# Kernel optimization log

Hardware: AMD Instinct MI355X
Metric: run time of the kernel (lower is better)

Reference implementation:

```python
import jax, jax.numpy as jnp
import numpy as np
from jax import lax

DIM = 64
BF = 2          # branching_factor
NUM_HEADS = 8
N_POS = 4096


def _expm(A, order=12, squarings=8):
    """Differentiable matrix exponential via scaling-and-squaring + Horner Taylor.
    Faithful substitute for torch.matrix_exp on skew-symmetric inputs."""
    d = A.shape[-1]
    I = jnp.eye(d, dtype=A.dtype)
    A = A / (2.0 ** squarings)
    E = I
    for k in range(order, 0, -1):
        E = I + jnp.matmul(A, E) / k
    for _ in range(squarings):
        E = jnp.matmul(E, E)
    return E


def _path_words_np(positions, bf):
    """Replicates create_paths + pad_sequence(padding_value=bf): tree path digits
    of node `pos` (root->leaf), right-padded with bf to the max actual length."""
    paths = []
    for p in positions:
        digs = []
        idx = int(p)
        while idx > 0:
            digs.append((idx - 1) % bf)
            idx = (idx - 1) // bf
        paths.append(digs[::-1] if p > 0 else [])
    T = max(1, max(len(p) for p in paths))
    out = np.full((len(paths), T), bf, dtype=np.int32)
    for i, p in enumerate(paths):
        out[i, :len(p)] = p
    return out


def setup_inputs() -> dict:
    key = jax.random.key(0)
    raw = jax.random.uniform(key, (BF * NUM_HEADS + 1, DIM, DIM), dtype=jnp.float32)
    # mimics torch.rand(...).softmax(-1).cumsum(-1) init of _primitives
    primitives_raw = jnp.cumsum(jax.nn.softmax(raw, axis=-1), axis=-1)
    positions = np.arange(N_POS)
    path_words = jnp.asarray(_path_words_np(positions, BF))  # [N, T] int32
    return {"primitives_raw": primitives_raw, "path_words": path_words}


def reference(primitives_raw, path_words):
    # primitives = matrix_exp(P - P^T)
    hermitian = primitives_raw - jnp.swapaxes(primitives_raw, -1, -2)
    primitives = _expm(hermitian)                      # [BF*H+1, d, d]
    d = primitives.shape[-1]
    I = jnp.eye(d, dtype=primitives.dtype)

    # linear(x, W) = x @ W.T; padding ids BF and BF+1 act as identity (no update)
    ext = jnp.concatenate(
        [jnp.swapaxes(primitives[:BF], -1, -2), jnp.broadcast_to(I, (2, d, d))],
        axis=0)                                        # [BF+2, d, d]

    n = path_words.shape[0]
    M0 = jnp.broadcast_to(I, (n, d, d))

    def body(M, w):  # w: [n] branch ids at this tree depth
        return jnp.einsum('nij,njk->nik', M, ext[w]), None

    M, _ = lax.scan(body, M0, path_words.T)            # fold over path depth
    maps = M[:, None]                                  # [n, 1, d, d]

    # create_steps: tree distance via common-prefix lengths
    pm = path_words != BF + 1                          # point mask [n, T]
    mask = pm[:, None, :] & pm[None, :, :]             # [n, n, T]
    eq = path_words[:, None, :] == path_words[None, :, :]
    common = lax.associative_scan(jnp.logical_and, eq, axis=-1) & mask
    lens = pm.sum(-1)
    steps = lens[:, None] + lens[None, :] - 2 * common.sum(-1).astype(lens.dtype)
    return maps, steps
```

## Files before the change

kernel.cpp:

```cpp
#include <hip/hip_runtime.h>


#define NPOS 4096
#define TLEN 12

typedef __attribute__((ext_vector_type(8))) short short8;
typedef __attribute__((ext_vector_type(4))) float f32x4;

__device__ __forceinline__ unsigned short f2bf(float f) {
  union { float f; unsigned u; } v; v.f = f;
  unsigned r = v.u + 0x7fffu + ((v.u >> 16) & 1u);
  return (unsigned short)(r >> 16);
}

__device__ __forceinline__ void mm64v(const float P[64][68], const float B[64][64],
                                      float acc[4][4], int r0, int c0) {
#pragma unroll 4
  for (int k0 = 0; k0 < 64; k0 += 4) {
    float a[4][4], bb[4][4];
#pragma unroll
    for (int i = 0; i < 4; ++i) {
      const float4 t = *reinterpret_cast<const float4*>(&P[r0 + i][k0]);
      a[i][0] = t.x; a[i][1] = t.y; a[i][2] = t.z; a[i][3] = t.w;
    }
#pragma unroll
    for (int kk = 0; kk < 4; ++kk) {
      const float4 t = *reinterpret_cast<const float4*>(&B[k0 + kk][c0]);
      bb[kk][0] = t.x; bb[kk][1] = t.y; bb[kk][2] = t.z; bb[kk][3] = t.w;
    }
#pragma unroll
    for (int i = 0; i < 4; ++i)
#pragma unroll
      for (int kk = 0; kk < 4; ++kk)
#pragma unroll
        for (int j = 0; j < 4; ++j) acc[i][j] += a[i][kk] * bb[kk][j];
  }
}

__device__ __forceinline__ float step_val(unsigned a, unsigned b) {
  const unsigned x = a ^ b;
  const int cp = x ? (__builtin_clz(x) >> 1) : TLEN;
  return (float)(2 * TLEN - 2 * cp);
}

__global__ __launch_bounds__(256) void expm_steps_kernel(
    const float* __restrict__ raw, const unsigned* __restrict__ keys,
    unsigned short* __restrict__ tabR, unsigned short* __restrict__ tabT,
    float* __restrict__ steps_out) {
  __shared__ float P[64][68];
  __shared__ float Bs[64][64];
  const int t = threadIdx.x;

  if (blockIdx.x >= 2) {
    const int b = (int)blockIdx.x - 2;
    const int i = b >> 2;
    const int j0 = ((b & 3) << 10) | (t << 2);
    const unsigned ki = keys[i];
    const uint4 kj = *reinterpret_cast<const uint4*>(&keys[j0]);
    float4 r;
    r.x = step_val(ki, kj.x);
    r.y = step_val(ki, kj.y);
    r.z = step_val(ki, kj.z);
    r.w = step_val(ki, kj.w);
    *reinterpret_cast<float4*>(&steps_out[(size_t)i * NPOS + j0]) = r;
    return;
  }

  const int d = blockIdx.x;
  const int r0 = (t >> 4) << 2, c0 = (t & 15) << 2;
#pragma unroll
  for (int i = 0; i < 16; ++i) {
    const int idx = (i << 8) | t;
    const int r = idx >> 6, c = idx & 63;
    const float a = (raw[d * 4096 + r * 64 + c] - raw[d * 4096 + c * 64 + r]) * (1.0f / 256.0f);
    P[r][c] = a;
    Bs[r][c] = ((r == c) ? 1.0f : 0.0f) + a * 0.2f;
  }
  __syncthreads();

  for (int k = 4; k >= 1; --k) {
    float acc[4][4] = {};
    mm64v(P, Bs, acc, r0, c0);
    __syncthreads();
    const float inv = 1.0f / (float)k;
#pragma unroll
    for (int i = 0; i < 4; ++i)
#pragma unroll
      for (int j = 0; j < 4; ++j) {
        const int r = r0 + i, c = c0 + j;
        Bs[r][c] = ((r == c) ? 1.0f : 0.0f) + acc[i][j] * inv;
      }
    __syncthreads();
  }

  for (int s = 0; s < 8; ++s) {
#pragma unroll
    for (int i = 0; i < 16; ++i) {
      const int idx = (i << 8) | t;
      P[idx >> 6][idx & 63] = Bs[idx >> 6][idx & 63];
    }
    __syncthreads();
    float acc[4][4] = {};
    mm64v(P, Bs, acc, r0, c0);
    __syncthreads();
#pragma unroll
    for (int i = 0; i < 4; ++i)
      *reinterpret_cast<float4*>(&Bs[r0 + i][c0]) =
          make_float4(acc[i][0], acc[i][1], acc[i][2], acc[i][3]);
    __syncthreads();
  }

  unsigned short* oR = tabR + (size_t)(1 + d) * 4096;
  unsigned short* oT = tabT + (size_t)(1 + d) * 4096;
#pragma unroll
  for (int i = 0; i < 16; ++i) {
    const int idx = (i << 8) | t;
    const int r = idx >> 6, c = idx & 63;
    oR[idx] = f2bf(Bs[c][r]);
    oT[idx] = f2bf(Bs[r][c]);
  }
  if (d == 0) {
#pragma unroll
    for (int i = 0; i < 16; ++i) {
      const int idx = (i << 8) | t;
      const int r = idx >> 6, c = idx & 63;
      const unsigned short v = (r == c) ? (unsigned short)0x3F80 : (unsigned short)0;
      tabR[idx] = v;
      tabT[idx] = v;
    }
  }
}

__device__ __forceinline__ void mfma64(const unsigned short* __restrict__ X,
                                       const unsigned short* __restrict__ Yt,
                                       f32x4 acc[4], int wv, int l) {
  const int row = l & 15, g = l >> 4;
  short8 a[2], b[4][2];
#pragma unroll
  for (int q = 0; q < 2; ++q)
    a[q] = *reinterpret_cast<const short8*>(X + (((16 * wv + row) << 6) | (q << 5) | (g << 3)));
#pragma unroll
  for (int c = 0; c < 4; ++c)
#pragma unroll
    for (int q = 0; q < 2; ++q)
      b[c][q] = *reinterpret_cast<const short8*>(Yt + (((16 * c + row) << 6) | (q << 5) | (g << 3)));
#pragma unroll
  for (int c = 0; c < 4; ++c) {
    acc[c] = __builtin_amdgcn_mfma_f32_16x16x32_bf16(a[0], b[c][0], acc[c], 0, 0, 0);
    acc[c] = __builtin_amdgcn_mfma_f32_16x16x32_bf16(a[1], b[c][1], acc[c], 0, 0, 0);
  }
}

__global__ __launch_bounds__(256) void pair_kernel(unsigned short* __restrict__ tabR,
                                                   unsigned short* __restrict__ tabT,
                                                   int mode) {
  const int bid = blockIdx.x;
  int xe, ye, oe;
  if (mode == 0) {
    xe = 1 + (bid >> 1); ye = 1 + (bid & 1); oe = 3 + bid;
  } else if (mode == 1) {
    if (bid < 8) { xe = 3 + (bid >> 1); ye = 1 + (bid & 1); oe = 7 + bid; }
    else { const int v = bid - 8; xe = 3 + (v >> 2); ye = 3 + (v & 3); oe = 15 + v; }
  } else {
    if (bid < 32) { xe = 15 + (bid >> 1); ye = 1 + (bid & 1); oe = 31 + bid; }
    else { const int v = bid - 32; xe = 15 + (v >> 2); ye = 3 + (v & 3); oe = 63 + v; }
  }
  const int wv = threadIdx.x >> 6, l = threadIdx.x & 63;
  f32x4 acc[4] = {f32x4{0,0,0,0}, f32x4{0,0,0,0}, f32x4{0,0,0,0}, f32x4{0,0,0,0}};
  mfma64(tabR + (size_t)xe * 4096, tabT + (size_t)ye * 4096, acc, wv, l);
  unsigned short* oR = tabR + (size_t)oe * 4096;
  unsigned short* oT = tabT + (size_t)oe * 4096;
  const int row = l & 15, g = l >> 4;
#pragma unroll
  for (int c = 0; c < 4; ++c)
#pragma unroll
    for (int r = 0; r < 4; ++r) {
      const unsigned short v = f2bf(acc[c][r]);
      const int rr = 16 * wv + 4 * g + r, cc = 16 * c + row;
      oR[rr * 64 + cc] = v;
      oT[cc * 64 + rr] = v;
    }
}

__global__ __launch_bounds__(256) void maps_kernel(const int* __restrict__ pw,
                                                   const unsigned short* __restrict__ tabR,
                                                   const unsigned short* __restrict__ tabT,
                                                   float* __restrict__ out) {
  const int n = blockIdx.x;
  int v1 = 0, l1 = 0, v2 = 0, l2 = 0;
#pragma unroll
  for (int tt = 0; tt < 6; ++tt) {
    const int w = pw[n * TLEN + tt];
    if (w < 2) { v1 = (v1 << 1) | w; ++l1; }
  }
#pragma unroll
  for (int tt = 6; tt < 12; ++tt) {
    const int w = pw[n * TLEN + tt];
    if (w < 2) { v2 = (v2 << 1) | w; ++l2; }
  }
  const int wv = threadIdx.x >> 6, l = threadIdx.x & 63;
  f32x4 acc[4] = {f32x4{0,0,0,0}, f32x4{0,0,0,0}, f32x4{0,0,0,0}, f32x4{0,0,0,0}};
  mfma64(tabR + (size_t)((1 << l1) - 1 + v1) * 4096,
         tabT + (size_t)((1 << l2) - 1 + v2) * 4096, acc, wv, l);
  float* O = out + (size_t)n * 4096;
  const int row = l & 15, g = l >> 4;
#pragma unroll
  for (int c = 0; c < 4; ++c)
#pragma unroll
    for (int r = 0; r < 4; ++r)
      O[((16 * wv + 4 * g + r) << 6) | (16 * c + row)] = acc[c][r];
}

__global__ __launch_bounds__(256) void keys_kernel(const int* __restrict__ pw,
                                                   unsigned* __restrict__ keys) {
  const int n = blockIdx.x * 256 + threadIdx.x;
  unsigned k = 0;
#pragma unroll
  for (int tt = 0; tt < TLEN; ++tt) k = (k << 2) | (unsigned)pw[n * TLEN + tt];
  keys[n] = k << 8;
}

extern "C" void kernel_launch(void* const* d_in, const int* in_sizes, int n_in,
                              void* d_out, int out_size, void* d_ws, size_t ws_size,
                              hipStream_t stream) {
  const float* raw = (const float*)d_in[0];
  const int* pw = (const int*)d_in[1];
  float* out = (float*)d_out;

  unsigned short* tabR = (unsigned short*)d_ws;
  unsigned short* tabT = tabR + (size_t)127 * 4096;
  unsigned* keys = (unsigned*)((char*)d_ws + (2u << 20));

  keys_kernel<<<NPOS / 256, 256, 0, stream>>>(pw, keys);
  expm_steps_kernel<<<2 + NPOS * 4, 256, 0, stream>>>(raw, keys, tabR, tabT,
                                                      out + (size_t)NPOS * 4096);
  pair_kernel<<<4, 256, 0, stream>>>(tabR, tabT, 0);
  pair_kernel<<<24, 256, 0, stream>>>(tabR, tabT, 1);
  pair_kernel<<<96, 256, 0, stream>>>(tabR, tabT, 2);
  maps_kernel<<<NPOS, 256, 0, stream>>>(pw, tabR, tabT, out);
}
```

Baseline: 185.5 us.

## Rework expm with Paterson-Stockmeyer, merge pair kernels, coalesce map stores

Several changes land together. The matrix exponential now uses fewer squarings (6 instead of 8) with a Paterson-Stockmeyer style evaluation of the degree-12 Taylor polynomial built from A and A^2, and uses packed float2 FMAs. The three level-by-level pair kernels become one 124-block kernel in which each block recomputes its own product chain from the two base primitives, which removes two launches and the inter-kernel dependency. The maps kernel stages its result in shared memory so it can write output with coalesced float4 stores. The serial expm chain and per-launch overhead are the targets, at the cost of redundant chained MFMA work in the pairs kernel and slightly changed numerics.

Result: slower. 199.1 us (+7.3%).

```diff
diff --git a/kernel.cpp b/kernel.cpp
--- a/kernel.cpp
+++ b/kernel.cpp
@@ -6,6 +6,7 @@
 
 typedef __attribute__((ext_vector_type(8))) short short8;
 typedef __attribute__((ext_vector_type(4))) float f32x4;
+typedef __attribute__((ext_vector_type(2))) float f32x2;
 
 __device__ __forceinline__ unsigned short f2bf(float f) {
   union { float f; unsigned u; } v; v.f = f;
@@ -13,27 +14,26 @@
   return (unsigned short)(r >> 16);
 }
 
-__device__ __forceinline__ void mm64v(const float P[64][68], const float B[64][64],
-                                      float acc[4][4], int r0, int c0) {
+__device__ __forceinline__ void mm64p(const float (*P)[68], const float (*B)[68],
+                                      f32x2 acc[4][2], int r0, int c0) {
 #pragma unroll 4
   for (int k0 = 0; k0 < 64; k0 += 4) {
-    float a[4][4], bb[4][4];
+    float a[4][4];
 #pragma unroll
     for (int i = 0; i < 4; ++i) {
-      const float4 t = *reinterpret_cast<const float4*>(&P[r0 + i][k0]);
-      a[i][0] = t.x; a[i][1] = t.y; a[i][2] = t.z; a[i][3] = t.w;
+      const float4 t4 = *reinterpret_cast<const float4*>(&P[r0 + i][k0]);
+      a[i][0] = t4.x; a[i][1] = t4.y; a[i][2] = t4.z; a[i][3] = t4.w;
     }
 #pragma unroll
     for (int kk = 0; kk < 4; ++kk) {
-      const float4 t = *reinterpret_cast<const float4*>(&B[k0 + kk][c0]);
-      bb[kk][0] = t.x; bb[kk][1] = t.y; bb[kk][2] = t.z; bb[kk][3] = t.w;
-    }
-#pragma unroll
-    for (int i = 0; i < 4; ++i)
-#pragma unroll
-      for (int kk = 0; kk < 4; ++kk)
-#pragma unroll
-        for (int j = 0; j < 4; ++j) acc[i][j] += a[i][kk] * bb[kk][j];
+      const float4 bv = *reinterpret_cast<const float4*>(&B[k0 + kk][c0]);
+      const f32x2 lo = {bv.x, bv.y}, hi = {bv.z, bv.w};
+#pragma unroll
+      for (int i = 0; i < 4; ++i) {
+        acc[i][0] += a[i][kk] * lo;
+        acc[i][1] += a[i][kk] * hi;
+      }
+    }
   }
 }
 
@@ -48,7 +48,7 @@
     unsigned short* __restrict__ tabR, unsigned short* __restrict__ tabT,
     float* __restrict__ steps_out) {
   __shared__ float P[64][68];
-  __shared__ float Bs[64][64];
+  __shared__ float Bs[64][68];
   const int t = threadIdx.x;
 
   if (blockIdx.x >= 2) {
@@ -68,57 +68,103 @@
 
   const int d = blockIdx.x;
   const int r0 = (t >> 4) << 2, c0 = (t & 15) << 2;
-#pragma unroll
-  for (int i = 0; i < 16; ++i) {
-    const int idx = (i << 8) | t;
-    const int r = idx >> 6, c = idx & 63;
-    const float a = (raw[d * 4096 + r * 64 + c] - raw[d * 4096 + c * 64 + r]) * (1.0f / 256.0f);
-    P[r][c] = a;
-    Bs[r][c] = ((r == c) ? 1.0f : 0.0f) + a * 0.2f;
-  }
-  __syncthreads();
-
-  for (int k = 4; k >= 1; --k) {
-    float acc[4][4] = {};
-    mm64v(P, Bs, acc, r0, c0);
-    __syncthreads();
-    const float inv = 1.0f / (float)k;
+  const float* R = raw + d * 4096;
+  float a_[4][4], a2_[4][4], e_[4][4];
+  f32x2 acc[4][2];
+#define ZACC { _Pragma("unroll") for (int i = 0; i < 4; ++i) { acc[i][0] = f32x2{0.f,0.f}; acc[i][1] = f32x2{0.f,0.f}; } }
+#define GETACC(i, j) ((j) < 2 ? acc[i][0][j] : acc[i][1][(j)-2])
+
+#pragma unroll
+  for (int i = 0; i < 4; ++i)
+#pragma unroll
+    for (int j = 0; j < 4; ++j)
+      a_[i][j] = (R[(r0 + i) * 64 + c0 + j] - R[(c0 + j) * 64 + r0 + i]) * (1.0f / 64.0f);
+#pragma unroll
+  for (int i = 0; i < 4; ++i) {
+    const float4 v = make_float4(a_[i][0], a_[i][1], a_[i][2], a_[i][3]);
+    *reinterpret_cast<float4*>(&P[r0 + i][c0]) = v;
+    *reinterpret_cast<float4*>(&Bs[r0 + i][c0]) = v;
+  }
+  __syncthreads();
+
+  ZACC; mm64p(P, Bs, acc, r0, c0);
+  __syncthreads();
+#pragma unroll
+  for (int i = 0; i < 4; ++i) {
+#pragma unroll
+    for (int j = 0; j < 4; ++j) a2_[i][j] = GETACC(i, j);
+    *reinterpret_cast<float4*>(&Bs[r0 + i][c0]) =
+        make_float4(a2_[i][0], a2_[i][1], a2_[i][2], a2_[i][3]);
+  }
+  __syncthreads();
+
+  ZACC; mm64p(P, Bs, acc, r0, c0);
+  __syncthreads();
+#pragma unroll
+  for (int i = 0; i < 4; ++i) {
+    float q[4];
+#pragma unroll
+    for (int j = 0; j < 4; ++j) {
+      const float id = (r0 + i == c0 + j) ? 1.0f : 0.0f;
+      q[j] = (1.0f / 362880.0f) * id + (1.0f / 3628800.0f) * a_[i][j] +
+             (1.0f / 39916800.0f) * a2_[i][j];
+    }
+    *reinterpret_cast<float4*>(&Bs[r0 + i][c0]) =
+        make_float4(GETACC(i, 0), GETACC(i, 1), GETACC(i, 2), GETACC(i, 3));
+    *reinterpret_cast<float4*>(&P[r0 + i][c0]) = make_float4(q[0], q[1], q[2], q[3]);
+  }
+  __syncthreads();
+
+  const float C[3][3] = {{1.0f / 720.0f, 1.0f / 5040.0f, 1.0f / 40320.0f},
+                         {1.0f / 6.0f, 1.0f / 24.0f, 1.0f / 120.0f},
+                         {1.0f, 1.0f, 0.5f}};
+#pragma unroll
+  for (int h = 0; h < 3; ++h) {
+    ZACC; mm64p(P, Bs, acc, r0, c0);
+    __syncthreads();
+#pragma unroll
+    for (int i = 0; i < 4; ++i) {
+      float q[4];
+#pragma unroll
+      for (int j = 0; j < 4; ++j) {
+        const float id = (r0 + i == c0 + j) ? 1.0f : 0.0f;
+        q[j] = GETACC(i, j) + C[h][0] * id + C[h][1] * a_[i][j] + C[h][2] * a2_[i][j];
+      }
+      const float4 v = make_float4(q[0], q[1], q[2], q[3]);
+      *reinterpret_cast<float4*>(&P[r0 + i][c0]) = v;
+      if (h == 2) *reinterpret_cast<float4*>(&Bs[r0 + i][c0]) = v;
+    }
+    __syncthreads();
+  }
+
+  for (int s = 0; s < 6; ++s) {
+    ZACC; mm64p(P, Bs, acc, r0, c0);
+    __syncthreads();
 #pragma unroll
     for (int i = 0; i < 4; ++i)
 #pragma unroll
-      for (int j = 0; j < 4; ++j) {
-        const int r = r0 + i, c = c0 + j;
-        Bs[r][c] = ((r == c) ? 1.0f : 0.0f) + acc[i][j] * inv;
+      for (int j = 0; j < 4; ++j) e_[i][j] = GETACC(i, j);
+    if (s < 5) {
+#pragma unroll
+      for (int i = 0; i < 4; ++i) {
+        const float4 v = make_float4(e_[i][0], e_[i][1], e_[i][2], e_[i][3]);
+        *reinterpret_cast<float4*>(&P[r0 + i][c0]) = v;
+        *reinterpret_cast<float4*>(&Bs[r0 + i][c0]) = v;
       }
-    __syncthreads();
-  }
-
-  for (int s = 0; s < 8; ++s) {
-#pragma unroll
-    for (int i = 0; i < 16; ++i) {
-      const int idx = (i << 8) | t;
-      P[idx >> 6][idx & 63] = Bs[idx >> 6][idx & 63];
-    }
-    __syncthreads();
-    float acc[4][4] = {};
-    mm64v(P, Bs, acc, r0, c0);
-    __syncthreads();
-#pragma unroll
-    for (int i = 0; i < 4; ++i)
-      *reinterpret_cast<float4*>(&Bs[r0 + i][c0]) =
-          make_float4(acc[i][0], acc[i][1], acc[i][2], acc[i][3]);
-    __syncthreads();
+      __syncthreads();
+    }
   }
 
   unsigned short* oR = tabR + (size_t)(1 + d) * 4096;
   unsigned short* oT = tabT + (size_t)(1 + d) * 4096;
 #pragma unroll
-  for (int i = 0; i < 16; ++i) {
-    const int idx = (i << 8) | t;
-    const int r = idx >> 6, c = idx & 63;
-    oR[idx] = f2bf(Bs[c][r]);
-    oT[idx] = f2bf(Bs[r][c]);
-  }
+  for (int i = 0; i < 4; ++i)
+#pragma unroll
+    for (int j = 0; j < 4; ++j) {
+      const unsigned short v = f2bf(e_[i][j]);
+      oR[(c0 + j) * 64 + (r0 + i)] = v;
+      oT[(r0 + i) * 64 + (c0 + j)] = v;
+    }
   if (d == 0) {
 #pragma unroll
     for (int i = 0; i < 16; ++i) {
@@ -129,6 +175,8 @@
       tabT[idx] = v;
     }
   }
+#undef ZACC
+#undef GETACC
 }
 
 __device__ __forceinline__ void mfma64(const unsigned short* __restrict__ X,
@@ -151,34 +199,70 @@
   }
 }
 
-__global__ __launch_bounds__(256) void pair_kernel(unsigned short* __restrict__ tabR,
-                                                   unsigned short* __restrict__ tabT,
-                                                   int mode) {
-  const int bid = blockIdx.x;
-  int xe, ye, oe;
-  if (mode == 0) {
-    xe = 1 + (bid >> 1); ye = 1 + (bid & 1); oe = 3 + bid;
-  } else if (mode == 1) {
-    if (bid < 8) { xe = 3 + (bid >> 1); ye = 1 + (bid & 1); oe = 7 + bid; }
-    else { const int v = bid - 8; xe = 3 + (v >> 2); ye = 3 + (v & 3); oe = 15 + v; }
-  } else {
-    if (bid < 32) { xe = 15 + (bid >> 1); ye = 1 + (bid & 1); oe = 31 + bid; }
-    else { const int v = bid - 32; xe = 15 + (v >> 2); ye = 3 + (v & 3); oe = 63 + v; }
-  }
+__global__ __launch_bounds__(256) void pairs_kernel(unsigned short* __restrict__ tabR,
+                                                    unsigned short* __restrict__ tabT) {
+  __shared__ unsigned short Tl[64][72];
+  const int e = 3 + (int)blockIdx.x;
+  const int lev = 31 - __clz(e + 1);
+  const int v = (e + 1) - (1 << lev);
   const int wv = threadIdx.x >> 6, l = threadIdx.x & 63;
+  const int row = l & 15, g = l >> 4;
+
+  short8 bT[2][4][2];
+#pragma unroll
+  for (int dd = 0; dd < 2; ++dd)
+#pragma unroll
+    for (int c = 0; c < 4; ++c)
+#pragma unroll
+      for (int q = 0; q < 2; ++q)
+        bT[dd][c][q] = *reinterpret_cast<const short8*>(
+            tabT + (size_t)(1 + dd) * 4096 + (((16 * c + row) << 6) | (q << 5) | (g << 3)));
+
+  const int d0 = (v >> (lev - 1)) & 1;
+  short8 a[2];
+#pragma unroll
+  for (int q = 0; q < 2; ++q)
+    a[q] = *reinterpret_cast<const short8*>(
+        tabR + (size_t)(1 + d0) * 4096 + (((16 * wv + row) << 6) | (q << 5) | (g << 3)));
+
   f32x4 acc[4] = {f32x4{0,0,0,0}, f32x4{0,0,0,0}, f32x4{0,0,0,0}, f32x4{0,0,0,0}};
-  mfma64(tabR + (size_t)xe * 4096, tabT + (size_t)ye * 4096, acc, wv, l);
-  unsigned short* oR = tabR + (size_t)oe * 4096;
-  unsigned short* oT = tabT + (size_t)oe * 4096;
-  const int row = l & 15, g = l >> 4;
+  const int d1 = (v >> (lev - 2)) & 1;
+#pragma unroll
+  for (int c = 0; c < 4; ++c) {
+    acc[c] = __builtin_amdgcn_mfma_f32_16x16x32_bf16(a[0], bT[d1][c][0], acc[c], 0, 0, 0);
+    acc[c] = __builtin_amdgcn_mfma_f32_16x16x32_bf16(a[1], bT[d1][c][1], acc[c], 0, 0, 0);
+  }
+
+  for (int j = 2; j < lev; ++j) {
+    const int dj = (v >> (lev - 1 - j)) & 1;
+#pragma unroll
+    for (int c = 0; c < 4; ++c)
+#pragma unroll
+      for (int r = 0; r < 4; ++r)
+        Tl[16 * wv + 4 * g + r][16 * c + row] = f2bf(acc[c][r]);
+    __syncthreads();
+#pragma unroll
+    for (int q = 0; q < 2; ++q)
+      a[q] = *reinterpret_cast<const short8*>(&Tl[16 * wv + row][(q << 5) | (g << 3)]);
+    __syncthreads();
+#pragma unroll
+    for (int c = 0; c < 4; ++c) {
+      acc[c] = f32x4{0, 0, 0, 0};
+      acc[c] = __builtin_amdgcn_mfma_f32_16x16x32_bf16(a[0], bT[dj][c][0], acc[c], 0, 0, 0);
+      acc[c] = __builtin_amdgcn_mfma_f32_16x16x32_bf16(a[1], bT[dj][c][1], acc[c], 0, 0, 0);
+    }
+  }
+
+  unsigned short* oR = tabR + (size_t)e * 4096;
+  unsigned short* oT = tabT + (size_t)e * 4096;
 #pragma unroll
   for (int c = 0; c < 4; ++c)
 #pragma unroll
     for (int r = 0; r < 4; ++r) {
-      const unsigned short v = f2bf(acc[c][r]);
+      const unsigned short val = f2bf(acc[c][r]);
       const int rr = 16 * wv + 4 * g + r, cc = 16 * c + row;
-      oR[rr * 64 + cc] = v;
-      oT[cc * 64 + rr] = v;
+      oR[rr * 64 + cc] = val;
+      oT[cc * 64 + rr] = val;
     }
 }
 
@@ -186,7 +270,9 @@
                                                    const unsigned short* __restrict__ tabR,
                                                    const unsigned short* __restrict__ tabT,
                                                    float* __restrict__ out) {
+  __shared__ float T[64][68];
   const int n = blockIdx.x;
+  const int t = threadIdx.x;
   int v1 = 0, l1 = 0, v2 = 0, l2 = 0;
 #pragma unroll
   for (int tt = 0; tt < 6; ++tt) {
@@ -198,17 +284,25 @@
     const int w = pw[n * TLEN + tt];
     if (w < 2) { v2 = (v2 << 1) | w; ++l2; }
   }
-  const int wv = threadIdx.x >> 6, l = threadIdx.x & 63;
+  const int wv = t >> 6, l = t & 63;
   f32x4 acc[4] = {f32x4{0,0,0,0}, f32x4{0,0,0,0}, f32x4{0,0,0,0}, f32x4{0,0,0,0}};
   mfma64(tabR + (size_t)((1 << l1) - 1 + v1) * 4096,
          tabT + (size_t)((1 << l2) - 1 + v2) * 4096, acc, wv, l);
+  const int row = l & 15, g = l >> 4;
+#pragma unroll
+  for (int c = 0; c < 4; ++c)
+#pragma unroll
+    for (int r = 0; r < 4; ++r)
+      T[16 * wv + 4 * g + r][16 * c + row] = acc[c][r];
+  __syncthreads();
   float* O = out + (size_t)n * 4096;
-  const int row = l & 15, g = l >> 4;
-#pragma unroll
-  for (int c = 0; c < 4; ++c)
-#pragma unroll
-    for (int r = 0; r < 4; ++r)
-      O[((16 * wv + 4 * g + r) << 6) | (16 * c + row)] = acc[c][r];
+#pragma unroll
+  for (int p = 0; p < 4; ++p) {
+    const int idx = (p << 8) | t;
+    const int rr = idx >> 4, cc = (idx & 15) << 2;
+    *reinterpret_cast<float4*>(&O[(rr << 6) | cc]) =
+        *reinterpret_cast<const float4*>(&T[rr][cc]);
+  }
 }
 
 __global__ __launch_bounds__(256) void keys_kernel(const int* __restrict__ pw,
@@ -229,13 +323,11 @@
 
   unsigned short* tabR = (unsigned short*)d_ws;
   unsigned short* tabT = tabR + (size_t)127 * 4096;
-  unsigned* keys = (unsigned*)((char*)d_ws + (2u << 20));
+  unsigned* keys = (unsigned*)((char*)d_ws + (4u << 20));
 
   keys_kernel<<<NPOS / 256, 256, 0, stream>>>(pw, keys);
   expm_steps_kernel<<<2 + NPOS * 4, 256, 0, stream>>>(raw, keys, tabR, tabT,
                                                       out + (size_t)NPOS * 4096);
-  pair_kernel<<<4, 256, 0, stream>>>(tabR, tabT, 0);
-  pair_kernel<<<24, 256, 0, stream>>>(tabR, tabT, 1);
-  pair_kernel<<<96, 256, 0, stream>>>(tabR, tabT, 2);
+  pairs_kernel<<<124, 256, 0, stream>>>(tabR, tabT);
   maps_kernel<<<NPOS, 256, 0, stream>>>(pw, tabR, tabT, out);
 }
```
